# Kernel optimization log

Hardware: AMD Instinct MI355X
Metric: run time of the kernel (lower is better)

## Reference

```python
import jax, jax.numpy as jnp
import numpy as np
from jax import lax

# ---- config (matches init_kwargs) ----
B, T, H = 4, 2048, 1024
HU = 4 * H                 # h_up = hidden*4
LAYERS, INDEX = 12, 0
K_CLAMP, K_EPS = 60.0, 1e-8
LN_EPS = 1e-5


def setup_inputs() -> dict:
    key = jax.random.key(0)
    ks = jax.random.split(key, 9)
    s = 0.02  # weight scale
    tr01 = INDEX / (LAYERS - 1)          # time_ratio_0_to_1
    tr1pz = 1.0 - INDEX / LAYERS         # time_ratio_1_to_pz
    i_h = np.arange(H, dtype=np.float64) / H
    i_hu = np.arange(HU, dtype=np.float64)
    # per-channel decay speed / first (sized to the WKV channel dim h_up)
    decay_speed = -5.0 + 8.0 * (i_hu / (HU - 1)) ** (0.7 + 1.3 * tr01)
    zigzag = ((np.arange(HU) + 1) % 3 - 1) * 0.5
    time_first = np.log(0.3) + zigzag
    f32 = lambda a: jnp.asarray(a, jnp.float32)
    return {
        "x": jax.random.normal(ks[0], (B, T, H), jnp.float32),
        "ln0_g": jnp.ones((H,), jnp.float32), "ln0_b": jnp.zeros((H,), jnp.float32),
        "pre_g": jnp.ones((H,), jnp.float32), "pre_b": jnp.zeros((H,), jnp.float32),
        "post_g": jnp.ones((H,), jnp.float32), "post_b": jnp.zeros((H,), jnp.float32),
        "tm_decay": f32(decay_speed),
        "tm_first": f32(time_first),
        "tm_mix_k": f32(i_h ** tr1pz),
        "tm_mix_v": f32(i_h ** tr1pz + 0.3 * tr01),
        "tm_mix_r": f32(i_h ** (0.5 * tr1pz)),
        "tm_Wk": jax.random.normal(ks[1], (H, HU), jnp.float32) * s,
        "tm_Wv": jax.random.normal(ks[2], (H, HU), jnp.float32) * s,
        "tm_Wr": jax.random.normal(ks[3], (H, HU), jnp.float32) * s,
        "tm_Wo": jax.random.normal(ks[4], (HU, H), jnp.float32) * s,
        "cm_mix_k": f32(i_h ** tr1pz),
        "cm_mix_r": f32(i_h ** tr1pz),
        "cm_Wk": jax.random.normal(ks[5], (H, HU), jnp.float32) * s,
        "cm_Wv": jax.random.normal(ks[6], (HU, H), jnp.float32) * s,
        "cm_Wr": jax.random.normal(ks[7], (H, H), jnp.float32) * s,
    }


def _ln(x, g, b):
    m = jnp.mean(x, -1, keepdims=True)
    v = jnp.mean((x - m) ** 2, -1, keepdims=True)
    return (x - m) / jnp.sqrt(v + LN_EPS) * g + b


def _shift(x):  # ZeroPad2d((0,0,1,-1)): xx[:, t] = x[:, t-1], xx[:, 0] = 0
    return jnp.pad(x[:, :-1], ((0, 0), (1, 0), (0, 0)))


def _wkv(k, kv, decay, first):
    # k, kv: [B, T, HU]; decay, first: [HU]
    # wkv[t] = first*kv[t] + sum_{d>=1} decay^(d-1) * kv[t-d]  (same for k)
    def step(carry, inp):
        sk, skv = carry
        kt, kvt = inp
        out = (first * kt + sk, first * kvt + skv)
        return (kt + decay * sk, kvt + decay * skv), out
    b = k.shape[0]
    init = (jnp.zeros((b, k.shape[2]), k.dtype), jnp.zeros((b, k.shape[2]), k.dtype))
    _, (wk, wkv) = lax.scan(step, init, (jnp.swapaxes(k, 0, 1), jnp.swapaxes(kv, 0, 1)))
    return jnp.swapaxes(wk, 0, 1), jnp.swapaxes(wkv, 0, 1)


def reference(x, ln0_g, ln0_b, pre_g, pre_b, post_g, post_b,
              tm_decay, tm_first, tm_mix_k, tm_mix_v, tm_mix_r,
              tm_Wk, tm_Wv, tm_Wr, tm_Wo,
              cm_mix_k, cm_mix_r, cm_Wk, cm_Wv, cm_Wr):
    if INDEX == 0:
        x = _ln(x, ln0_g, ln0_b)

    # ---- RWKV_TM (time mix / WKV) ----
    xn = _ln(x, pre_g, pre_b)
    xx = _shift(xn)
    xk = xn * tm_mix_k + xx * (1.0 - tm_mix_k)
    xv = xn * tm_mix_v + xx * (1.0 - tm_mix_v)
    xr = xn * tm_mix_r + xx * (1.0 - tm_mix_r)
    k = jnp.exp(jnp.minimum(xk @ tm_Wk, K_CLAMP))   # [B,T,HU]
    v = xv @ tm_Wv                                  # [B,T,HU]
    r = xr @ tm_Wr                                  # [B,T,HU]
    kv = k * v
    decay = jnp.exp(-jnp.exp(tm_decay))  # per-step multiplier exp(-exp(time_decay))
    first = jnp.exp(tm_first)
    wk, wkv = _wkv(k, kv, decay, first)
    rwkv = jax.nn.sigmoid(r) * (wkv / (wk + K_EPS))
    x = x + rwkv @ tm_Wo

    # ---- RWKV_CM (channel mix) ----
    xn = _ln(x, post_g, post_b)
    xx = _shift(xn)
    xk = xn * cm_mix_k + xx * (1.0 - cm_mix_k)
    xr = xn * cm_mix_r + xx * (1.0 - cm_mix_r)
    kv = jax.nn.silu(xk @ cm_Wk) @ cm_Wv            # [B,T,H]
    x = x + (jax.nn.sigmoid(xr @ cm_Wr) + kv)
    return x
```

## Files before the change

### kernel.cpp

```cpp
#include <hip/hip_runtime.h>

#define Hdim  1024
#define Tdim  2048
#define Bdim  4
#define HUdim 4096
#define Mrows (Bdim*Tdim)
#define CHUNK 2048
#define NCH   (HUdim/CHUNK)
#define NSEG  16
#define SEGL  (Tdim/NSEG)
#define SCHUNK 16

typedef __bf16 bf16;
typedef __bf16 bf16x8 __attribute__((ext_vector_type(8)));
typedef float  floatx4 __attribute__((ext_vector_type(4)));

__device__ __forceinline__ bf16 f2bf(float x) { return (bf16)x; }

__global__ __launch_bounds__(256) void wconv_all(
    const float* __restrict__ s0, const float* __restrict__ s1, const float* __restrict__ s2,
    const float* __restrict__ s3, const float* __restrict__ s4, const float* __restrict__ s5,
    const float* __restrict__ s6,
    bf16* d0, bf16* d1, bf16* d2, bf16* d3, bf16* d4, bf16* d5, bf16* d6) {
  __shared__ float tile[64][65];
  int bid = blockIdx.x;
  const float* src; bf16* dst; int K, N, local;
  if (bid < 1024)      { src = s0; dst = d0; K = Hdim;  N = HUdim; local = bid; }
  else if (bid < 2048) { src = s1; dst = d1; K = Hdim;  N = HUdim; local = bid - 1024; }
  else if (bid < 3072) { src = s2; dst = d2; K = Hdim;  N = HUdim; local = bid - 2048; }
  else if (bid < 4096) { src = s3; dst = d3; K = HUdim; N = Hdim;  local = bid - 3072; }
  else if (bid < 5120) { src = s4; dst = d4; K = Hdim;  N = HUdim; local = bid - 4096; }
  else if (bid < 6144) { src = s5; dst = d5; K = HUdim; N = Hdim;  local = bid - 5120; }
  else                 { src = s6; dst = d6; K = Hdim;  N = Hdim;  local = bid - 6144; }
  const int nt = N >> 6;
  const int n0 = (local % nt) * 64, k0 = (local / nt) * 64;
  const int tr = threadIdx.x >> 6;
  const int tc = threadIdx.x & 63;
#pragma unroll
  for (int j = 0; j < 16; j++) {
    int r = j * 4 + tr;
    tile[r][tc] = src[(size_t)(k0 + r) * N + n0 + tc];
  }
  __syncthreads();
#pragma unroll
  for (int j = 0; j < 16; j++) {
    int r = j * 4 + tr;
    dst[(size_t)(n0 + r) * K + k0 + tc] = f2bf(tile[tc][r]);
  }
}

__device__ __forceinline__ void block_reduce4(float v[4], float* sm) {
#pragma unroll
  for (int off = 32; off > 0; off >>= 1) {
#pragma unroll
    for (int i = 0; i < 4; i++) v[i] += __shfl_down(v[i], off, 64);
  }
  const int w = threadIdx.x >> 6;
  if ((threadIdx.x & 63) == 0) {
#pragma unroll
    for (int i = 0; i < 4; i++) sm[w * 4 + i] = v[i];
  }
  __syncthreads();
#pragma unroll
  for (int i = 0; i < 4; i++) v[i] = sm[i] + sm[4 + i] + sm[8 + i] + sm[12 + i];
  __syncthreads();
}

__global__ __launch_bounds__(256) void ln_mix_tm(
    const float* __restrict__ x,
    const float* __restrict__ g0, const float* __restrict__ b0,
    const float* __restrict__ g1, const float* __restrict__ b1,
    const float* __restrict__ mk, const float* __restrict__ mv, const float* __restrict__ mr,
    float* __restrict__ x0, bf16* __restrict__ xk, bf16* __restrict__ xv, bf16* __restrict__ xr) {
  __shared__ float sm[16];
  const int bid = blockIdx.x;
  const int t = bid & (Tdim - 1);
  const int tid = threadIdx.x;
  const bool havep = (t > 0);
  const float hp = havep ? 1.f : 0.f;
  const float* rowc = x + (size_t)bid * Hdim;
  const float* rowp = havep ? (rowc - Hdim) : rowc;

  float c[4], p[4];
#pragma unroll
  for (int j = 0; j < 4; j++) c[j] = rowc[tid * 4 + j];
#pragma unroll
  for (int j = 0; j < 4; j++) p[j] = rowp[tid * 4 + j] * hp;

  float red[4] = {0.f, 0.f, 0.f, 0.f};
#pragma unroll
  for (int j = 0; j < 4; j++) { red[0] += c[j]; red[1] += c[j]*c[j]; red[2] += p[j]; red[3] += p[j]*p[j]; }
  block_reduce4(red, sm);
  const float inv = 1.f / Hdim;
  float mc = red[0]*inv, vc = red[1]*inv - mc*mc;
  float mp = red[2]*inv, vp = red[3]*inv - mp*mp;
  float sc = rsqrtf(vc + 1e-5f), sp = rsqrtf(vp + 1e-5f);

  float yc[4], yp[4];
#pragma unroll
  for (int j = 0; j < 4; j++) {
    int i = tid * 4 + j;
    yc[j] = (c[j] - mc) * sc * g0[i] + b0[i];
    yp[j] = ((p[j] - mp) * sp * g0[i] + b0[i]) * hp;
    x0[(size_t)bid * Hdim + i] = yc[j];
  }

  float r2[4] = {0.f, 0.f, 0.f, 0.f};
#pragma unroll
  for (int j = 0; j < 4; j++) { r2[0] += yc[j]; r2[1] += yc[j]*yc[j]; r2[2] += yp[j]; r2[3] += yp[j]*yp[j]; }
  block_reduce4(r2, sm);
  float mc2 = r2[0]*inv, vc2 = r2[1]*inv - mc2*mc2;
  float mp2 = r2[2]*inv, vp2 = r2[3]*inv - mp2*mp2;
  float sc2 = rsqrtf(vc2 + 1e-5f), sp2 = rsqrtf(vp2 + 1e-5f);

#pragma unroll
  for (int j = 0; j < 4; j++) {
    int i = tid * 4 + j;
    float xnc = (yc[j] - mc2) * sc2 * g1[i] + b1[i];
    float xnp = ((yp[j] - mp2) * sp2 * g1[i] + b1[i]) * hp;
    size_t o = (size_t)bid * Hdim + i;
    float a;
    a = mk[i]; xk[o] = f2bf(xnc * a + xnp * (1.f - a));
    a = mv[i]; xv[o] = f2bf(xnc * a + xnp * (1.f - a));
    a = mr[i]; xr[o] = f2bf(xnc * a + xnp * (1.f - a));
  }
}

__global__ __launch_bounds__(256) void ln_mix_cm(
    const float* __restrict__ xin,
    const float* __restrict__ g, const float* __restrict__ bb,
    const float* __restrict__ mk, const float* __restrict__ mr,
    bf16* __restrict__ xk, bf16* __restrict__ xr) {
  __shared__ float sm[16];
  const int bid = blockIdx.x;
  const int t = bid & (Tdim - 1);
  const int tid = threadIdx.x;
  const bool havep = (t > 0);
  const float hp = havep ? 1.f : 0.f;
  const float* rowc = xin + (size_t)bid * Hdim;
  const float* rowp = havep ? (rowc - Hdim) : rowc;

  float c[4], p[4];
#pragma unroll
  for (int j = 0; j < 4; j++) c[j] = rowc[tid * 4 + j];
#pragma unroll
  for (int j = 0; j < 4; j++) p[j] = rowp[tid * 4 + j] * hp;

  float red[4] = {0.f, 0.f, 0.f, 0.f};
#pragma unroll
  for (int j = 0; j < 4; j++) { red[0] += c[j]; red[1] += c[j]*c[j]; red[2] += p[j]; red[3] += p[j]*p[j]; }
  block_reduce4(red, sm);
  const float inv = 1.f / Hdim;
  float mc = red[0]*inv, vc = red[1]*inv - mc*mc;
  float mp = red[2]*inv, vp = red[3]*inv - mp*mp;
  float sc = rsqrtf(vc + 1e-5f), sp = rsqrtf(vp + 1e-5f);

#pragma unroll
  for (int j = 0; j < 4; j++) {
    int i = tid * 4 + j;
    float xnc = (c[j] - mc) * sc * g[i] + bb[i];
    float xnp = ((p[j] - mp) * sp * g[i] + bb[i]) * hp;
    size_t o = (size_t)bid * Hdim + i;
    float a;
    a = mk[i]; xk[o] = f2bf(xnc * a + xnp * (1.f - a));
    a = mr[i]; xr[o] = f2bf(xnc * a + xnp * (1.f - a));
  }
}

__global__ __launch_bounds__(64) void wkv_part(
    const bf16* __restrict__ Kb, const bf16* __restrict__ Vb,
    float* __restrict__ stK, float* __restrict__ stKV,
    const float* __restrict__ tdec) {
  const int seg = blockIdx.x & (NSEG - 1);
  const int rest = blockIdx.x >> 4;
  const int b = rest >> 5, g = rest & 31;
  const int c = (g << 6) + threadIdx.x;
  const float decay = __expf(-__expf(tdec[c]));
  size_t base = ((size_t)b * Tdim + (size_t)seg * SEGL) * CHUNK + c;
  float sk = 0.f, skv = 0.f;
  for (int t0 = 0; t0 < SEGL; t0 += SCHUNK) {
    float kk[SCHUNK], vv[SCHUNK];
#pragma unroll
    for (int j = 0; j < SCHUNK; j++) {
      size_t idx = base + (size_t)(t0 + j) * CHUNK;
      kk[j] = (float)Kb[idx];
      vv[j] = (float)Vb[idx];
    }
#pragma unroll
    for (int j = 0; j < SCHUNK; j++) {
      float kvt = kk[j] * vv[j];
      sk  = fmaf(decay, sk, kk[j]);
      skv = fmaf(decay, skv, kvt);
    }
  }
  size_t so = ((size_t)seg * Bdim + b) * CHUNK + c;
  stK[so]  = sk;
  stKV[so] = skv;
}

__global__ __launch_bounds__(64) void wkv_emit(
    const bf16* __restrict__ Kb, const bf16* __restrict__ Vb,
    const bf16* SRb, bf16* Pb,
    const float* __restrict__ stK, const float* __restrict__ stKV,
    const float* __restrict__ tdec, const float* __restrict__ tfst) {
  const int seg = blockIdx.x & (NSEG - 1);
  const int rest = blockIdx.x >> 4;
  const int b = rest >> 5, g = rest & 31;
  const int c = (g << 6) + threadIdx.x;
  const float ed = __expf(tdec[c]);
  const float decay = __expf(-ed);
  const float dfac  = __expf(-ed * (float)SEGL);
  const float first = __expf(tfst[c]);

  float sk = 0.f, skv = 0.f;
  for (int j = 0; j < seg; j++) {
    size_t so = ((size_t)j * Bdim + b) * CHUNK + c;
    sk  = fmaf(dfac, sk, stK[so]);
    skv = fmaf(dfac, skv, stKV[so]);
  }

  size_t base = ((size_t)b * Tdim + (size_t)seg * SEGL) * CHUNK + c;
  for (int t0 = 0; t0 < SEGL; t0 += SCHUNK) {
    float kk[SCHUNK], vv[SCHUNK], rr[SCHUNK];
#pragma unroll
    for (int j = 0; j < SCHUNK; j++) {
      size_t idx = base + (size_t)(t0 + j) * CHUNK;
      kk[j] = (float)Kb[idx];
      vv[j] = (float)Vb[idx];
      rr[j] = (float)SRb[idx];
    }
#pragma unroll
    for (int j = 0; j < SCHUNK; j++) {
      size_t idx = base + (size_t)(t0 + j) * CHUNK;
      float kvt = kk[j] * vv[j];
      float wk  = fmaf(first, kk[j], sk) + 1e-8f;
      float wkv = fmaf(first, kvt, skv);
      Pb[idx] = f2bf(rr[j] * wkv * __builtin_amdgcn_rcpf(wk));
      sk  = fmaf(decay, sk, kk[j]);
      skv = fmaf(decay, skv, kvt);
    }
  }
}

__device__ __forceinline__ void gld_lds(const bf16* g, bf16* l) {
  __builtin_amdgcn_global_load_lds(
      (const __attribute__((address_space(1))) void*)(g),
      (__attribute__((address_space(3))) void*)(l),
      16, 0, 0);
}

__device__ __forceinline__ void swz(int s, int gm, int& m_t, int& n_t) {
  const int mpx  = gm >> 3;
  const int xcd  = s & 7;
  const int ss   = s >> 3;
  const int pass = mpx << 1;
  const int ng   = ss / pass;
  const int rem  = ss - ng * pass;
  m_t = xcd * mpx + (rem >> 1);
  n_t = (ng << 1) + (rem & 1);
}

__device__ __forceinline__ void mm_core64(
    const bf16* A, const bf16* Bt, int lda, int ldb, int K,
    long m0, long n0, int wv, int lane, int wm, int wn,
    bf16* As, bf16* Bs, floatx4 acc[4][4]) {
  const int srow = wv * 32 + (lane >> 2);
  const int scol = (((lane & 3) - ((lane >> 3) & 3)) & 3) * 8;
  const bf16* gA = A + (m0 + srow) * (long)lda + scol;
  const bf16* gB = Bt + (n0 + srow) * (long)ldb + scol;
  const long skipA = 16L * lda;
  const long skipB = 16L * ldb;
  bf16* lA = As + wv * 1024;
  bf16* lB = Bs + wv * 1024;
  const int pg = ((lane >> 4) + ((lane >> 1) & 3)) & 3;
  const bf16* fa = As + ((wm * 64) + (lane & 15)) * 32 + pg * 8;
  const bf16* fb = Bs + ((wn * 64) + (lane & 15)) * 32 + pg * 8;

  const int ksteps = K >> 6;
  for (int kt = 0; kt < ksteps; ++kt) {
    __syncthreads();
    gld_lds(gA, lA);             gld_lds(gA + skipA, lA + 512);
    gld_lds(gA + 32, lA + 4096); gld_lds(gA + 32 + skipA, lA + 4096 + 512);
    gld_lds(gB, lB);             gld_lds(gB + skipB, lB + 512);
    gld_lds(gB + 32, lB + 4096); gld_lds(gB + 32 + skipB, lB + 4096 + 512);
    gA += 64; gB += 64;
    __syncthreads();
#pragma unroll
    for (int s = 0; s < 2; s++) {
      bf16x8 af[4], bfr[4];
#pragma unroll
      for (int i = 0; i < 4; i++) {
        af[i]  = *(const bf16x8*)(fa + s * 4096 + i * 512);
        bfr[i] = *(const bf16x8*)(fb + s * 4096 + i * 512);
      }
#pragma unroll
      for (int mt = 0; mt < 4; mt++)
#pragma unroll
        for (int nt = 0; nt < 4; nt++)
          acc[mt][nt] = __builtin_amdgcn_mfma_f32_16x16x32_bf16(af[mt], bfr[nt], acc[mt][nt], 0, 0, 0);
    }
  }
}

enum { E_EXP = 0, E_BF16 = 1, E_SIG = 2, E_ADD1 = 3, E_SILU = 4, E_F32 = 5, E_SIGADD2 = 6 };

template <int EPI>
__global__ __launch_bounds__(256) void gemm_bt(
    const bf16* __restrict__ A, const bf16* __restrict__ Bt,
    void* Cout, const void* aux1, const void* aux2,
    int lda, int ldb, int ldc, int K, int gm, int gn) {
  __shared__ __align__(16) bf16 As[2 * 128 * 32];
  __shared__ __align__(16) bf16 Bs[2 * 128 * 32];
  const int tid = threadIdx.x;
  const int lane = tid & 63;
  const int wv = tid >> 6;
  const int wm = wv >> 1, wn = wv & 1;
  int m_t, n_t;
  swz(blockIdx.x, gm, m_t, n_t);
  const long m0 = (long)m_t * 128;
  const long n0 = (long)n_t * 128;

  floatx4 acc[4][4];
#pragma unroll
  for (int i = 0; i < 4; i++)
#pragma unroll
    for (int j = 0; j < 4; j++) acc[i][j] = (floatx4){0.f, 0.f, 0.f, 0.f};

  mm_core64(A, Bt, lda, ldb, K, m0, n0, wv, lane, wm, wn, As, Bs, acc);

  const int r0 = wm * 64 + ((lane >> 4) << 2);
  const int c0 = wn * 64 + (lane & 15);
#pragma unroll
  for (int mt = 0; mt < 4; mt++) {
#pragma unroll
    for (int i = 0; i < 4; i++) {
      long r = m0 + r0 + mt * 16 + i;
      long bidx = r * (long)ldc + n0 + c0;
#pragma unroll
      for (int nt = 0; nt < 4; nt++) {
        long idx = bidx + nt * 16;
        float v = acc[mt][nt][i];
        if constexpr (EPI == E_EXP) {
          ((bf16*)Cout)[idx] = f2bf(__expf(fminf(v, 60.f)));
        } else if constexpr (EPI == E_BF16) {
          ((bf16*)Cout)[idx] = f2bf(v);
        } else if constexpr (EPI == E_SIG) {
          ((bf16*)Cout)[idx] = f2bf(1.f / (1.f + __expf(-v)));
        } else if constexpr (EPI == E_ADD1) {
          float prev = ((const float*)aux1)[idx];
          ((float*)Cout)[idx] = v + prev;
        } else if constexpr (EPI == E_SILU) {
          ((bf16*)Cout)[idx] = f2bf(v / (1.f + __expf(-v)));
        } else if constexpr (EPI == E_F32) {
          ((float*)Cout)[idx] = v;
        } else {
          float a1 = ((const float*)aux1)[idx];
          float a2 = ((const float*)aux2)[idx];
          ((float*)Cout)[idx] = a1 + 1.f / (1.f + __expf(-v)) + a2;
        }
      }
    }
  }
}

__global__ __launch_bounds__(256) void proj3(
    const bf16* __restrict__ xk, const bf16* __restrict__ xv, const bf16* __restrict__ xr,
    const bf16* __restrict__ Wk, const bf16* __restrict__ Wv, const bf16* __restrict__ Wr,
    bf16* Kc, bf16* Vc, bf16* SRc, int gm, int gn) {
  __shared__ __align__(16) bf16 As[2 * 128 * 32];
  __shared__ __align__(16) bf16 Bs[2 * 128 * 32];
  const int per = gm * gn;
  const int sub = blockIdx.x / per;
  const int s   = blockIdx.x - sub * per;
  const int tid = threadIdx.x;
  const int lane = tid & 63;
  const int wv = tid >> 6;
  const int wm = wv >> 1, wn = wv & 1;
  int m_t, n_t;
  swz(s, gm, m_t, n_t);
  const long m0 = (long)m_t * 128;
  const long n0 = (long)n_t * 128;

  const bf16* A  = (sub == 0) ? xk : (sub == 1) ? xv : xr;
  const bf16* Bt = (sub == 0) ? Wk : (sub == 1) ? Wv : Wr;
  bf16*       C  = (sub == 0) ? Kc : (sub == 1) ? Vc : SRc;

  floatx4 acc[4][4];
#pragma unroll
  for (int i = 0; i < 4; i++)
#pragma unroll
    for (int j = 0; j < 4; j++) acc[i][j] = (floatx4){0.f, 0.f, 0.f, 0.f};

  mm_core64(A, Bt, Hdim, Hdim, Hdim, m0, n0, wv, lane, wm, wn, As, Bs, acc);

  const int r0 = wm * 64 + ((lane >> 4) << 2);
  const int c0 = wn * 64 + (lane & 15);
#pragma unroll
  for (int mt = 0; mt < 4; mt++) {
#pragma unroll
    for (int i = 0; i < 4; i++) {
      long r = m0 + r0 + mt * 16 + i;
      long bidx = r * (long)CHUNK + n0 + c0;
#pragma unroll
      for (int nt = 0; nt < 4; nt++) {
        long idx = bidx + nt * 16;
        float v = acc[mt][nt][i];
        float o;
        if (sub == 0)      o = __expf(fminf(v, 60.f));
        else if (sub == 1) o = v;
        else               o = 1.f / (1.f + __expf(-v));
        C[idx] = f2bf(o);
      }
    }
  }
}

extern "C" void kernel_launch(void* const* d_in, const int* in_sizes, int n_in,
                              void* d_out, int out_size, void* d_ws, size_t ws_size,
                              hipStream_t stream) {
  (void)in_sizes; (void)n_in; (void)out_size; (void)ws_size;
  const float* x        = (const float*)d_in[0];
  const float* ln0_g    = (const float*)d_in[1];
  const float* ln0_b    = (const float*)d_in[2];
  const float* pre_g    = (const float*)d_in[3];
  const float* pre_b    = (const float*)d_in[4];
  const float* post_g   = (const float*)d_in[5];
  const float* post_b   = (const float*)d_in[6];
  const float* tm_decay = (const float*)d_in[7];
  const float* tm_first = (const float*)d_in[8];
  const float* tm_mix_k = (const float*)d_in[9];
  const float* tm_mix_v = (const float*)d_in[10];
  const float* tm_mix_r = (const float*)d_in[11];
  const float* tm_Wk    = (const float*)d_in[12];
  const float* tm_Wv    = (const float*)d_in[13];
  const float* tm_Wr    = (const float*)d_in[14];
  const float* tm_Wo    = (const float*)d_in[15];
  const float* cm_mix_k = (const float*)d_in[16];
  const float* cm_mix_r = (const float*)d_in[17];
  const float* cm_Wk    = (const float*)d_in[18];
  const float* cm_Wv    = (const float*)d_in[19];
  const float* cm_Wr    = (const float*)d_in[20];

  char* ws = (char*)d_ws;
  bf16*  WkT  = (bf16*)(ws + 0);
  bf16*  WvT  = (bf16*)(ws + 8388608);
  bf16*  WrT  = (bf16*)(ws + 16777216);
  bf16*  WoT  = (bf16*)(ws + 25165824);
  bf16*  cWkT = (bf16*)(ws + 33554432);
  bf16*  cWvT = (bf16*)(ws + 41943040);
  bf16*  cWrT = (bf16*)(ws + 50331648);
  float* xres = (float*)(ws + 52428800);
  bf16*  xk   = (bf16*)(ws + 85983232);
  bf16*  xv   = (bf16*)(ws + 102760448);
  bf16*  xr   = (bf16*)(ws + 119537664);
  bf16*  Kc   = (bf16*)(ws + 136314880);
  bf16*  Vc   = (bf16*)(ws + 169869312);
  bf16*  SRc  = (bf16*)(ws + 203423744);
  float* stK  = (float*)(ws + 236978176);
  float* stKV = (float*)(ws + 237502464);
  bf16*  xk2  = (bf16*)(ws + 136314880);
  bf16*  xr2  = (bf16*)(ws + 153092096);
  bf16*  hbuf = (bf16*)(ws + 169869312);
  float* hv   = (float*)(ws + 85983232);

  dim3 blk(256);
  wconv_all<<<6400, blk, 0, stream>>>(tm_Wk, tm_Wv, tm_Wr, tm_Wo, cm_Wk, cm_Wv, cm_Wr,
                                      WkT, WvT, WrT, WoT, cWkT, cWvT, cWrT);

  ln_mix_tm<<<Mrows, blk, 0, stream>>>(x, ln0_g, ln0_b, pre_g, pre_b,
                                       tm_mix_k, tm_mix_v, tm_mix_r, xres, xk, xv, xr);

  const int scan_grid = NSEG * Bdim * (CHUNK / 64);
  const int GM = Mrows / 128;
  const int GNp = CHUNK / 128;
  for (int ch = 0; ch < NCH; ch++) {
    const long woff = (long)ch * CHUNK;
    proj3<<<3 * GM * GNp, blk, 0, stream>>>(
        xk, xv, xr, WkT + woff * Hdim, WvT + woff * Hdim, WrT + woff * Hdim,
        Kc, Vc, SRc, GM, GNp);

    wkv_part<<<scan_grid, dim3(64), 0, stream>>>(
        Kc, Vc, stK, stKV, tm_decay + woff);
    wkv_emit<<<scan_grid, dim3(64), 0, stream>>>(
        Kc, Vc, SRc, SRc, stK, stKV, tm_decay + woff, tm_first + woff);

    gemm_bt<E_ADD1><<<GM * (Hdim/128), blk, 0, stream>>>(
        SRc, WoT + woff, xres, xres, nullptr, CHUNK, HUdim, Hdim, CHUNK, GM, Hdim/128);
  }

  ln_mix_cm<<<Mrows, blk, 0, stream>>>(xres, post_g, post_b, cm_mix_k, cm_mix_r, xk2, xr2);

  gemm_bt<E_SILU><<<GM * (HUdim/128), blk, 0, stream>>>(
      xk2, cWkT, hbuf, nullptr, nullptr, Hdim, Hdim, HUdim, Hdim, GM, HUdim/128);

  gemm_bt<E_F32><<<GM * (Hdim/128), blk, 0, stream>>>(
      hbuf, cWvT, hv, nullptr, nullptr, HUdim, HUdim, Hdim, CHUNK, GM, Hdim/128);
  gemm_bt<E_ADD1><<<GM * (Hdim/128), blk, 0, stream>>>(
      hbuf + CHUNK, cWvT + CHUNK, hv, hv, nullptr, HUdim, HUdim, Hdim, CHUNK, GM, Hdim/128);

  gemm_bt<E_SIGADD2><<<GM * (Hdim/128), blk, 0, stream>>>(
      xr2, cWrT, (float*)d_out, xres, hv, Hdim, Hdim, Hdim, Hdim, GM, Hdim/128);
}
```

Before: 994.2 us.

## Vectorize WKV scans to two channels per thread and loop GEMM blocks over two M tiles

```diff
diff --git a/kernel.cpp b/kernel.cpp
--- a/kernel.cpp
+++ b/kernel.cpp
@@ -12,6 +12,7 @@
 #define SCHUNK 16
 
 typedef __bf16 bf16;
+typedef __bf16 bf16x2 __attribute__((ext_vector_type(2)));
 typedef __bf16 bf16x8 __attribute__((ext_vector_type(8)));
 typedef float  floatx4 __attribute__((ext_vector_type(4)));
 
@@ -173,29 +174,31 @@
     const float* __restrict__ tdec) {
   const int seg = blockIdx.x & (NSEG - 1);
   const int rest = blockIdx.x >> 4;
-  const int b = rest >> 5, g = rest & 31;
-  const int c = (g << 6) + threadIdx.x;
-  const float decay = __expf(-__expf(tdec[c]));
+  const int b = rest >> 4, g = rest & 15;
+  const int c = (g << 7) + (threadIdx.x << 1);
+  const float d0 = __expf(-__expf(tdec[c]));
+  const float d1 = __expf(-__expf(tdec[c + 1]));
   size_t base = ((size_t)b * Tdim + (size_t)seg * SEGL) * CHUNK + c;
-  float sk = 0.f, skv = 0.f;
+  float sk0 = 0.f, skv0 = 0.f, sk1 = 0.f, skv1 = 0.f;
   for (int t0 = 0; t0 < SEGL; t0 += SCHUNK) {
-    float kk[SCHUNK], vv[SCHUNK];
+    bf16x2 kk[SCHUNK], vv[SCHUNK];
 #pragma unroll
     for (int j = 0; j < SCHUNK; j++) {
       size_t idx = base + (size_t)(t0 + j) * CHUNK;
-      kk[j] = (float)Kb[idx];
-      vv[j] = (float)Vb[idx];
+      kk[j] = *(const bf16x2*)(Kb + idx);
+      vv[j] = *(const bf16x2*)(Vb + idx);
     }
 #pragma unroll
     for (int j = 0; j < SCHUNK; j++) {
-      float kvt = kk[j] * vv[j];
-      sk  = fmaf(decay, sk, kk[j]);
-      skv = fmaf(decay, skv, kvt);
+      float k0 = (float)kk[j][0], k1 = (float)kk[j][1];
+      float v0 = (float)vv[j][0], v1 = (float)vv[j][1];
+      sk0  = fmaf(d0, sk0, k0);   skv0 = fmaf(d0, skv0, k0 * v0);
+      sk1  = fmaf(d1, sk1, k1);   skv1 = fmaf(d1, skv1, k1 * v1);
     }
   }
   size_t so = ((size_t)seg * Bdim + b) * CHUNK + c;
-  stK[so]  = sk;
-  stKV[so] = skv;
+  stK[so]      = sk0;  stK[so + 1]  = sk1;
+  stKV[so]     = skv0; stKV[so + 1] = skv1;
 }
 
 __global__ __launch_bounds__(64) void wkv_emit(
@@ -205,39 +208,47 @@
     const float* __restrict__ tdec, const float* __restrict__ tfst) {
   const int seg = blockIdx.x & (NSEG - 1);
   const int rest = blockIdx.x >> 4;
-  const int b = rest >> 5, g = rest & 31;
-  const int c = (g << 6) + threadIdx.x;
-  const float ed = __expf(tdec[c]);
-  const float decay = __expf(-ed);
-  const float dfac  = __expf(-ed * (float)SEGL);
-  const float first = __expf(tfst[c]);
-
-  float sk = 0.f, skv = 0.f;
+  const int b = rest >> 4, g = rest & 15;
+  const int c = (g << 7) + (threadIdx.x << 1);
+  const float ed0 = __expf(tdec[c]),     ed1 = __expf(tdec[c + 1]);
+  const float d0  = __expf(-ed0),        d1  = __expf(-ed1);
+  const float df0 = __expf(-ed0 * (float)SEGL);
+  const float df1 = __expf(-ed1 * (float)SEGL);
+  const float f0  = __expf(tfst[c]),     f1  = __expf(tfst[c + 1]);
+
+  float sk0 = 0.f, skv0 = 0.f, sk1 = 0.f, skv1 = 0.f;
   for (int j = 0; j < seg; j++) {
     size_t so = ((size_t)j * Bdim + b) * CHUNK + c;
-    sk  = fmaf(dfac, sk, stK[so]);
-    skv = fmaf(dfac, skv, stKV[so]);
+    sk0  = fmaf(df0, sk0,  stK[so]);      sk1  = fmaf(df1, sk1,  stK[so + 1]);
+    skv0 = fmaf(df0, skv0, stKV[so]);     skv1 = fmaf(df1, skv1, stKV[so + 1]);
   }
 
   size_t base = ((size_t)b * Tdim + (size_t)seg * SEGL) * CHUNK + c;
   for (int t0 = 0; t0 < SEGL; t0 += SCHUNK) {
-    float kk[SCHUNK], vv[SCHUNK], rr[SCHUNK];
+    bf16x2 kk[SCHUNK], vv[SCHUNK], rr[SCHUNK];
 #pragma unroll
     for (int j = 0; j < SCHUNK; j++) {
       size_t idx = base + (size_t)(t0 + j) * CHUNK;
-      kk[j] = (float)Kb[idx];
-      vv[j] = (float)Vb[idx];
-      rr[j] = (float)SRb[idx];
+      kk[j] = *(const bf16x2*)(Kb + idx);
+      vv[j] = *(const bf16x2*)(Vb + idx);
+      rr[j] = *(const bf16x2*)(SRb + idx);
     }
 #pragma unroll
     for (int j = 0; j < SCHUNK; j++) {
       size_t idx = base + (size_t)(t0 + j) * CHUNK;
-      float kvt = kk[j] * vv[j];
-      float wk  = fmaf(first, kk[j], sk) + 1e-8f;
-      float wkv = fmaf(first, kvt, skv);
-      Pb[idx] = f2bf(rr[j] * wkv * __builtin_amdgcn_rcpf(wk));
-      sk  = fmaf(decay, sk, kk[j]);
-      skv = fmaf(decay, skv, kvt);
+      float k0 = (float)kk[j][0], k1 = (float)kk[j][1];
+      float v0 = (float)vv[j][0], v1 = (float)vv[j][1];
+      float kv0 = k0 * v0, kv1 = k1 * v1;
+      float wk0  = fmaf(f0, k0, sk0) + 1e-8f;
+      float wk1  = fmaf(f1, k1, sk1) + 1e-8f;
+      float wkv0 = fmaf(f0, kv0, skv0);
+      float wkv1 = fmaf(f1, kv1, skv1);
+      bf16x2 out;
+      out[0] = f2bf((float)rr[j][0] * wkv0 * __builtin_amdgcn_rcpf(wk0));
+      out[1] = f2bf((float)rr[j][1] * wkv1 * __builtin_amdgcn_rcpf(wk1));
+      *(bf16x2*)(Pb + idx) = out;
+      sk0  = fmaf(d0, sk0, k0);   skv0 = fmaf(d0, skv0, kv0);
+      sk1  = fmaf(d1, sk1, k1);   skv1 = fmaf(d1, skv1, kv1);
     }
   }
 }
@@ -305,29 +316,9 @@
 enum { E_EXP = 0, E_BF16 = 1, E_SIG = 2, E_ADD1 = 3, E_SILU = 4, E_F32 = 5, E_SIGADD2 = 6 };
 
 template <int EPI>
-__global__ __launch_bounds__(256) void gemm_bt(
-    const bf16* __restrict__ A, const bf16* __restrict__ Bt,
-    void* Cout, const void* aux1, const void* aux2,
-    int lda, int ldb, int ldc, int K, int gm, int gn) {
-  __shared__ __align__(16) bf16 As[2 * 128 * 32];
-  __shared__ __align__(16) bf16 Bs[2 * 128 * 32];
-  const int tid = threadIdx.x;
-  const int lane = tid & 63;
-  const int wv = tid >> 6;
-  const int wm = wv >> 1, wn = wv & 1;
-  int m_t, n_t;
-  swz(blockIdx.x, gm, m_t, n_t);
-  const long m0 = (long)m_t * 128;
-  const long n0 = (long)n_t * 128;
-
-  floatx4 acc[4][4];
-#pragma unroll
-  for (int i = 0; i < 4; i++)
-#pragma unroll
-    for (int j = 0; j < 4; j++) acc[i][j] = (floatx4){0.f, 0.f, 0.f, 0.f};
-
-  mm_core64(A, Bt, lda, ldb, K, m0, n0, wv, lane, wm, wn, As, Bs, acc);
-
+__device__ __forceinline__ void epilogue(
+    floatx4 acc[4][4], void* Cout, const void* aux1, const void* aux2,
+    long m0, long n0, int ldc, int lane, int wm, int wn) {
   const int r0 = wm * 64 + ((lane >> 4) << 2);
   const int c0 = wn * 64 + (lane & 15);
 #pragma unroll
@@ -363,6 +354,34 @@
   }
 }
 
+template <int EPI, int MT>
+__global__ __launch_bounds__(256) void gemm_bt(
+    const bf16* __restrict__ A, const bf16* __restrict__ Bt,
+    void* Cout, const void* aux1, const void* aux2,
+    int lda, int ldb, int ldc, int K, int gm, int gn) {
+  __shared__ __align__(16) bf16 As[2 * 128 * 32];
+  __shared__ __align__(16) bf16 Bs[2 * 128 * 32];
+  const int tid = threadIdx.x;
+  const int lane = tid & 63;
+  const int wv = tid >> 6;
+  const int wm = wv >> 1, wn = wv & 1;
+  int m_t, n_t;
+  swz(blockIdx.x, gm, m_t, n_t);
+  const long n0 = (long)n_t * 128;
+
+#pragma unroll
+  for (int sm = 0; sm < MT; sm++) {
+    const long m0 = (long)m_t * (128 * MT) + sm * 128;
+    floatx4 acc[4][4];
+#pragma unroll
+    for (int i = 0; i < 4; i++)
+#pragma unroll
+      for (int j = 0; j < 4; j++) acc[i][j] = (floatx4){0.f, 0.f, 0.f, 0.f};
+    mm_core64(A, Bt, lda, ldb, K, m0, n0, wv, lane, wm, wn, As, Bs, acc);
+    epilogue<EPI>(acc, Cout, aux1, aux2, m0, n0, ldc, lane, wm, wn);
+  }
+}
+
 __global__ __launch_bounds__(256) void proj3(
     const bf16* __restrict__ xk, const bf16* __restrict__ xv, const bf16* __restrict__ xr,
     const bf16* __restrict__ Wk, const bf16* __restrict__ Wv, const bf16* __restrict__ Wr,
@@ -378,38 +397,40 @@
   const int wm = wv >> 1, wn = wv & 1;
   int m_t, n_t;
   swz(s, gm, m_t, n_t);
-  const long m0 = (long)m_t * 128;
   const long n0 = (long)n_t * 128;
 
   const bf16* A  = (sub == 0) ? xk : (sub == 1) ? xv : xr;
   const bf16* Bt = (sub == 0) ? Wk : (sub == 1) ? Wv : Wr;
   bf16*       C  = (sub == 0) ? Kc : (sub == 1) ? Vc : SRc;
 
-  floatx4 acc[4][4];
-#pragma unroll
-  for (int i = 0; i < 4; i++)
-#pragma unroll
-    for (int j = 0; j < 4; j++) acc[i][j] = (floatx4){0.f, 0.f, 0.f, 0.f};
-
-  mm_core64(A, Bt, Hdim, Hdim, Hdim, m0, n0, wv, lane, wm, wn, As, Bs, acc);
-
-  const int r0 = wm * 64 + ((lane >> 4) << 2);
-  const int c0 = wn * 64 + (lane & 15);
-#pragma unroll
-  for (int mt = 0; mt < 4; mt++) {
-#pragma unroll
-    for (int i = 0; i < 4; i++) {
-      long r = m0 + r0 + mt * 16 + i;
-      long bidx = r * (long)CHUNK + n0 + c0;
-#pragma unroll
-      for (int nt = 0; nt < 4; nt++) {
-        long idx = bidx + nt * 16;
-        float v = acc[mt][nt][i];
-        float o;
-        if (sub == 0)      o = __expf(fminf(v, 60.f));
-        else if (sub == 1) o = v;
-        else               o = 1.f / (1.f + __expf(-v));
-        C[idx] = f2bf(o);
+#pragma unroll
+  for (int sm = 0; sm < 2; sm++) {
+    const long m0 = (long)m_t * 256 + sm * 128;
+    floatx4 acc[4][4];
+#pragma unroll
+    for (int i = 0; i < 4; i++)
+#pragma unroll
+      for (int j = 0; j < 4; j++) acc[i][j] = (floatx4){0.f, 0.f, 0.f, 0.f};
+    mm_core64(A, Bt, Hdim, Hdim, Hdim, m0, n0, wv, lane, wm, wn, As, Bs, acc);
+
+    const int r0 = wm * 64 + ((lane >> 4) << 2);
+    const int c0 = wn * 64 + (lane & 15);
+#pragma unroll
+    for (int mt = 0; mt < 4; mt++) {
+#pragma unroll
+      for (int i = 0; i < 4; i++) {
+        long r = m0 + r0 + mt * 16 + i;
+        long bidx = r * (long)CHUNK + n0 + c0;
+#pragma unroll
+        for (int nt = 0; nt < 4; nt++) {
+          long idx = bidx + nt * 16;
+          float v = acc[mt][nt][i];
+          float o;
+          if (sub == 0)      o = __expf(fminf(v, 60.f));
+          else if (sub == 1) o = v;
+          else               o = 1.f / (1.f + __expf(-v));
+          C[idx] = f2bf(o);
+        }
       }
     }
   }
@@ -470,34 +491,35 @@
   ln_mix_tm<<<Mrows, blk, 0, stream>>>(x, ln0_g, ln0_b, pre_g, pre_b,
                                        tm_mix_k, tm_mix_v, tm_mix_r, xres, xk, xv, xr);
 
-  const int scan_grid = NSEG * Bdim * (CHUNK / 64);
+  const int scan_grid = NSEG * Bdim * (CHUNK / 128);
   const int GM = Mrows / 128;
+  const int GM2 = Mrows / 256;
   const int GNp = CHUNK / 128;
   for (int ch = 0; ch < NCH; ch++) {
     const long woff = (long)ch * CHUNK;
-    proj3<<<3 * GM * GNp, blk, 0, stream>>>(
+    proj3<<<3 * GM2 * GNp, blk, 0, stream>>>(
         xk, xv, xr, WkT + woff * Hdim, WvT + woff * Hdim, WrT + woff * Hdim,
-        Kc, Vc, SRc, GM, GNp);
+        Kc, Vc, SRc, GM2, GNp);
 
     wkv_part<<<scan_grid, dim3(64), 0, stream>>>(
         Kc, Vc, stK, stKV, tm_decay + woff);
     wkv_emit<<<scan_grid, dim3(64), 0, stream>>>(
         Kc, Vc, SRc, SRc, stK, stKV, tm_decay + woff, tm_first + woff);
 
-    gemm_bt<E_ADD1><<<GM * (Hdim/128), blk, 0, stream>>>(
+    gemm_bt<E_ADD1, 1><<<GM * (Hdim/128), blk, 0, stream>>>(
         SRc, WoT + woff, xres, xres, nullptr, CHUNK, HUdim, Hdim, CHUNK, GM, Hdim/128);
   }
 
   ln_mix_cm<<<Mrows, blk, 0, stream>>>(xres, post_g, post_b, cm_mix_k, cm_mix_r, xk2, xr2);
 
-  gemm_bt<E_SILU><<<GM * (HUdim/128), blk, 0, stream>>>(
-      xk2, cWkT, hbuf, nullptr, nullptr, Hdim, Hdim, HUdim, Hdim, GM, HUdim/128);
-
-  gemm_bt<E_F32><<<GM * (Hdim/128), blk, 0, stream>>>(
+  gemm_bt<E_SILU, 2><<<GM2 * (HUdim/128), blk, 0, stream>>>(
+      xk2, cWkT, hbuf, nullptr, nullptr, Hdim, Hdim, HUdim, Hdim, GM2, HUdim/128);
+
+  gemm_bt<E_F32, 1><<<GM * (Hdim/128), blk, 0, stream>>>(
       hbuf, cWvT, hv, nullptr, nullptr, HUdim, HUdim, Hdim, CHUNK, GM, Hdim/128);
-  gemm_bt<E_ADD1><<<GM * (Hdim/128), blk, 0, stream>>>(
+  gemm_bt<E_ADD1, 1><<<GM * (Hdim/128), blk, 0, stream>>>(
       hbuf + CHUNK, cWvT + CHUNK, hv, hv, nullptr, HUdim, HUdim, Hdim, CHUNK, GM, Hdim/128);
 
-  gemm_bt<E_SIGADD2><<<GM * (Hdim/128), blk, 0, stream>>>(
+  gemm_bt<E_SIGADD2, 1><<<GM * (Hdim/128), blk, 0, stream>>>(
       xr2, cWrT, (float*)d_out, xres, hv, Hdim, Hdim, Hdim, Hdim, GM, Hdim/128);
 }
```

New measurement: 987.9 us. No clear change (-0.6%).
